# Kernel tuning notes

Hardware: AMD Instinct MI355X
Metric: run time of the kernel (lower is better)

## Reference

```python
import jax, jax.numpy as jnp
import numpy as np
from jax import lax

KSIZE = 3
SIGMA = 0.3 * ((KSIZE - 1) * 0.5 - 1) + 0.8  # cv2 auto-sigma for k=3 -> 0.8

def _gauss_kernel(k, sigma):
    ax = np.arange(k, dtype=np.float64) - (k - 1) / 2
    xx, yy = np.meshgrid(ax, ax, indexing='ij')
    ker = np.exp(-(xx ** 2 + yy ** 2) / (2.0 * sigma ** 2))
    ker /= ker.sum()
    return jnp.asarray(ker, jnp.float32)

SCHARR_X = jnp.array([[-3., 0., 3.], [-10., 0., 10.], [-3., 0., 3.]], jnp.float32)
SCHARR_Y = SCHARR_X.T  # cv2.Scharr(dy=1)

def _conv2d_reflect(img, ker):
    # img: [B,1,H,W]; cross-correlation (like cv2.filter2D) with BORDER_REFLECT_101
    p = ker.shape[0] // 2
    img = jnp.pad(img, ((0, 0), (0, 0), (p, p), (p, p)), mode='reflect')
    return lax.conv_general_dilated(img, ker[None, None], (1, 1), 'VALID')

def setup_inputs() -> dict:
    key = jax.random.key(0)
    x = jax.random.uniform(key, (8, 3, 1024, 1024), dtype=jnp.float32) * 255.0
    return {"x": x}

def reference(x):
    B, C, H, W = x.shape
    # cv2 RGB2GRAY weights
    rgb_w = jnp.array([0.299, 0.587, 0.114], dtype=x.dtype)
    gray = jnp.einsum('bchw,c->bhw', x, rgb_w)[:, None]  # [B,1,H,W]
    blurred = _conv2d_reflect(gray, _gauss_kernel(KSIZE, SIGMA))
    sx = _conv2d_reflect(blurred, SCHARR_X)
    sy = _conv2d_reflect(blurred, SCHARR_Y)
    mag = jnp.sqrt(sx * sx + sy * sy)  # L2_gradient=True
    # forward returns gradient magnitude replicated across channels
    return jnp.broadcast_to(mag, (B, C, H, W))
```

## Files before the change

### kernel.cpp

```cpp
#include <hip/hip_runtime.h>
#include <math.h>


#define IMG_H 1024
#define IMG_W 1024
#define TW 128
#define TH 16
#define GCOLS 136
#define ITEMS 768

#define W0 0.52201125f
#define W1 0.23899437f
#define AV0 0.71698311f
#define AV1 3.95597745f
#define AV2 6.65407872f

typedef float vf4 __attribute__((ext_vector_type(4)));
#define AS_GLOBAL const __attribute__((address_space(1))) void*
#define AS_LDS __attribute__((address_space(3))) void*

__device__ __forceinline__ int reflect101(int v, int n) {
    v = (v < 0) ? -v : v;
    return (v >= n) ? (2 * n - 2 - v) : v;
}

__global__ __launch_bounds__(256, 4)
void edge_kernel(const float* __restrict__ in, float* __restrict__ out) {
    __shared__ __align__(16) float sR[ITEMS * 4];
    __shared__ __align__(16) float sG[ITEMS * 4];
    __shared__ __align__(16) float sB[ITEMS * 4];

    const int tid = threadIdx.x;
    const int bx = blockIdx.x, by = blockIdx.y, b = blockIdx.z;
    const int x0 = bx * TW, y0 = by * TH;

    const size_t plane = (size_t)IMG_H * IMG_W;
    const float* pr = in + (size_t)b * 3 * plane;
    const float* pg = pr + plane;
    const float* pb = pg + plane;

    #pragma unroll
    for (int k = 0; k < 3; ++k) {
        const int item = tid + k * 256;
        const int gy = item / 34;
        const int g4 = (item - gy * 34) * 4;
        const int y = reflect101(y0 - 2 + gy, IMG_H);
        int x = x0 - 4 + g4;
        x = x < 0 ? 0 : (x > IMG_W - 4 ? IMG_W - 4 : x);
        const size_t o = (size_t)y * IMG_W + x;
        __builtin_amdgcn_global_load_lds((AS_GLOBAL)(pr + o), (AS_LDS)&sR[item * 4], 16, 0, 0);
        __builtin_amdgcn_global_load_lds((AS_GLOBAL)(pg + o), (AS_LDS)&sG[item * 4], 16, 0, 0);
        __builtin_amdgcn_global_load_lds((AS_GLOBAL)(pb + o), (AS_LDS)&sB[item * 4], 16, 0, 0);
    }
    __syncthreads();

    #pragma unroll
    for (int k = 0; k < 3; ++k) {
        const int i4 = (tid + k * 256) * 4;
        float4 r = *(const float4*)&sR[i4];
        float4 g = *(const float4*)&sG[i4];
        float4 bb = *(const float4*)&sB[i4];
        float4 gr;
        gr.x = 0.299f * r.x + 0.587f * g.x + 0.114f * bb.x;
        gr.y = 0.299f * r.y + 0.587f * g.y + 0.114f * bb.y;
        gr.z = 0.299f * r.z + 0.587f * g.z + 0.114f * bb.z;
        gr.w = 0.299f * r.w + 0.587f * g.w + 0.114f * bb.w;
        *(float4*)&sR[i4] = gr;
    }
    __syncthreads();

    const int tx = tid & 31;
    const int tyg = tid >> 5;
    const int c4 = tx * 4;
    const int r0 = tyg * 2;
    const bool eBL = (bx == 0) && (tx == 0);
    const bool eBR = (bx == (IMG_W / TW - 1)) && (tx == 31);

    float hs[6][4], hd[6][4];
    #pragma unroll
    for (int s = 0; s < 6; ++s) {
        const float* row = &sR[(r0 + s) * GCOLS + c4];
        float4 ga = *(const float4*)(row);
        float4 gb = *(const float4*)(row + 4);
        float4 gc = *(const float4*)(row + 8);
        float g[12] = {ga.x, ga.y, ga.z, ga.w, gb.x, gb.y, gb.z, gb.w,
                       gc.x, gc.y, gc.z, gc.w};
        if (eBL) { g[2] = g[6]; g[3] = g[5]; }
        if (eBR) { g[8] = g[6]; g[9] = g[5]; }
        #pragma unroll
        for (int k = 0; k < 4; ++k) {
            hs[s][k] = AV0 * (g[k+2] + g[k+6]) + AV1 * (g[k+3] + g[k+5]) + AV2 * g[k+4];
            hd[s][k] = W1 * (g[k+6] - g[k+2]) + W0 * (g[k+5] - g[k+3]);
        }
    }

    float* po = out + (size_t)b * 3 * plane;
    #pragma unroll
    for (int t = 0; t < 2; ++t) {
        vf4 mag;
        #pragma unroll
        for (int k = 0; k < 4; ++k) {
            float sx = AV0 * (hd[t][k] + hd[t+4][k]) + AV1 * (hd[t+1][k] + hd[t+3][k]) + AV2 * hd[t+2][k];
            float sy = W1 * (hs[t+4][k] - hs[t][k]) + W0 * (hs[t+3][k] - hs[t+1][k]);
            mag[k] = sqrtf(sx * sx + sy * sy);
        }
        const size_t o = (size_t)(y0 + r0 + t) * IMG_W + (x0 + c4);
        __builtin_nontemporal_store(mag, (vf4*)(po + o));
        __builtin_nontemporal_store(mag, (vf4*)(po + o + plane));
        __builtin_nontemporal_store(mag, (vf4*)(po + o + 2 * plane));
    }
}

extern "C" void kernel_launch(void* const* d_in, const int* in_sizes, int n_in,
                              void* d_out, int out_size, void* d_ws, size_t ws_size,
                              hipStream_t stream) {
    const float* in = (const float*)d_in[0];
    float* out = (float*)d_out;
    const int B = in_sizes[0] / (3 * IMG_H * IMG_W);
    dim3 grid(IMG_W / TW, IMG_H / TH, B);
    edge_kernel<<<grid, dim3(256), 0, stream>>>(in, out);
}
```

Before: 175.4 us.

## Make blocks persistent over 8 row tiles with double-buffered async LDS staging

```diff
diff --git a/kernel.cpp b/kernel.cpp
--- a/kernel.cpp
+++ b/kernel.cpp
@@ -6,6 +6,7 @@
 #define IMG_W 1024
 #define TW 128
 #define TH 16
+#define NT 8
 #define GCOLS 136
 #define ITEMS 768
 
@@ -24,50 +25,36 @@
     return (v >= n) ? (2 * n - 2 - v) : v;
 }
 
-__global__ __launch_bounds__(256, 4)
+__global__ __launch_bounds__(256, 2)
 void edge_kernel(const float* __restrict__ in, float* __restrict__ out) {
-    __shared__ __align__(16) float sR[ITEMS * 4];
-    __shared__ __align__(16) float sG[ITEMS * 4];
-    __shared__ __align__(16) float sB[ITEMS * 4];
+    __shared__ __align__(16) float sAll[2][3][ITEMS * 4];
 
     const int tid = threadIdx.x;
-    const int bx = blockIdx.x, by = blockIdx.y, b = blockIdx.z;
-    const int x0 = bx * TW, y0 = by * TH;
+    const int bx = blockIdx.x, sy = blockIdx.y, b = blockIdx.z;
+    const int x0 = bx * TW;
+    const int ybase = sy * (TH * NT);
 
     const size_t plane = (size_t)IMG_H * IMG_W;
     const float* pr = in + (size_t)b * 3 * plane;
     const float* pg = pr + plane;
     const float* pb = pg + plane;
+    float* po = out + (size_t)b * 3 * plane;
 
-    #pragma unroll
-    for (int k = 0; k < 3; ++k) {
-        const int item = tid + k * 256;
-        const int gy = item / 34;
-        const int g4 = (item - gy * 34) * 4;
-        const int y = reflect101(y0 - 2 + gy, IMG_H);
-        int x = x0 - 4 + g4;
-        x = x < 0 ? 0 : (x > IMG_W - 4 ? IMG_W - 4 : x);
-        const size_t o = (size_t)y * IMG_W + x;
-        __builtin_amdgcn_global_load_lds((AS_GLOBAL)(pr + o), (AS_LDS)&sR[item * 4], 16, 0, 0);
-        __builtin_amdgcn_global_load_lds((AS_GLOBAL)(pg + o), (AS_LDS)&sG[item * 4], 16, 0, 0);
-        __builtin_amdgcn_global_load_lds((AS_GLOBAL)(pb + o), (AS_LDS)&sB[item * 4], 16, 0, 0);
-    }
-    __syncthreads();
-
-    #pragma unroll
-    for (int k = 0; k < 3; ++k) {
-        const int i4 = (tid + k * 256) * 4;
-        float4 r = *(const float4*)&sR[i4];
-        float4 g = *(const float4*)&sG[i4];
-        float4 bb = *(const float4*)&sB[i4];
-        float4 gr;
-        gr.x = 0.299f * r.x + 0.587f * g.x + 0.114f * bb.x;
-        gr.y = 0.299f * r.y + 0.587f * g.y + 0.114f * bb.y;
-        gr.z = 0.299f * r.z + 0.587f * g.z + 0.114f * bb.z;
-        gr.w = 0.299f * r.w + 0.587f * g.w + 0.114f * bb.w;
-        *(float4*)&sR[i4] = gr;
-    }
-    __syncthreads();
+    auto STAGE = [&](int bufi, int ty0) {
+        #pragma unroll
+        for (int k = 0; k < 3; ++k) {
+            const int item = tid + k * 256;
+            const int gy = item / 34;
+            const int g4 = (item - gy * 34) * 4;
+            const int y = reflect101(ty0 - 2 + gy, IMG_H);
+            int x = x0 - 4 + g4;
+            x = x < 0 ? 0 : (x > IMG_W - 4 ? IMG_W - 4 : x);
+            const size_t o = (size_t)y * IMG_W + x;
+            __builtin_amdgcn_global_load_lds((AS_GLOBAL)(pr + o), (AS_LDS)&sAll[bufi][0][item * 4], 16, 0, 0);
+            __builtin_amdgcn_global_load_lds((AS_GLOBAL)(pg + o), (AS_LDS)&sAll[bufi][1][item * 4], 16, 0, 0);
+            __builtin_amdgcn_global_load_lds((AS_GLOBAL)(pb + o), (AS_LDS)&sAll[bufi][2][item * 4], 16, 0, 0);
+        }
+    };
 
     const int tx = tid & 31;
     const int tyg = tid >> 5;
@@ -76,38 +63,70 @@
     const bool eBL = (bx == 0) && (tx == 0);
     const bool eBR = (bx == (IMG_W / TW - 1)) && (tx == 31);
 
-    float hs[6][4], hd[6][4];
+    STAGE(0, ybase);
+
     #pragma unroll
-    for (int s = 0; s < 6; ++s) {
-        const float* row = &sR[(r0 + s) * GCOLS + c4];
-        float4 ga = *(const float4*)(row);
-        float4 gb = *(const float4*)(row + 4);
-        float4 gc = *(const float4*)(row + 8);
-        float g[12] = {ga.x, ga.y, ga.z, ga.w, gb.x, gb.y, gb.z, gb.w,
-                       gc.x, gc.y, gc.z, gc.w};
-        if (eBL) { g[2] = g[6]; g[3] = g[5]; }
-        if (eBR) { g[8] = g[6]; g[9] = g[5]; }
+    for (int t = 0; t < NT; ++t) {
+        const int cur = t & 1;
+        if (t < NT - 1) STAGE(cur ^ 1, ybase + (t + 1) * TH);
+
+        if (t == 0)            asm volatile("s_waitcnt vmcnt(9)"  ::: "memory");
+        else if (t == NT - 1)  asm volatile("s_waitcnt vmcnt(6)"  ::: "memory");
+        else                   asm volatile("s_waitcnt vmcnt(15)" ::: "memory");
+
         #pragma unroll
-        for (int k = 0; k < 4; ++k) {
-            hs[s][k] = AV0 * (g[k+2] + g[k+6]) + AV1 * (g[k+3] + g[k+5]) + AV2 * g[k+4];
-            hd[s][k] = W1 * (g[k+6] - g[k+2]) + W0 * (g[k+5] - g[k+3]);
+        for (int k = 0; k < 3; ++k) {
+            const int i4 = (tid + k * 256) * 4;
+            float4 r  = *(const float4*)&sAll[cur][0][i4];
+            float4 g  = *(const float4*)&sAll[cur][1][i4];
+            float4 bb = *(const float4*)&sAll[cur][2][i4];
+            float4 gr;
+            gr.x = 0.299f * r.x + 0.587f * g.x + 0.114f * bb.x;
+            gr.y = 0.299f * r.y + 0.587f * g.y + 0.114f * bb.y;
+            gr.z = 0.299f * r.z + 0.587f * g.z + 0.114f * bb.z;
+            gr.w = 0.299f * r.w + 0.587f * g.w + 0.114f * bb.w;
+            *(float4*)&sAll[cur][0][i4] = gr;
         }
-    }
+        asm volatile("s_waitcnt lgkmcnt(0)" ::: "memory");
+        __builtin_amdgcn_s_barrier();
+        __builtin_amdgcn_sched_barrier(0);
 
-    float* po = out + (size_t)b * 3 * plane;
-    #pragma unroll
-    for (int t = 0; t < 2; ++t) {
-        vf4 mag;
+        const int ty0 = ybase + t * TH;
+        float hs[6][4], hd[6][4];
         #pragma unroll
-        for (int k = 0; k < 4; ++k) {
-            float sx = AV0 * (hd[t][k] + hd[t+4][k]) + AV1 * (hd[t+1][k] + hd[t+3][k]) + AV2 * hd[t+2][k];
-            float sy = W1 * (hs[t+4][k] - hs[t][k]) + W0 * (hs[t+3][k] - hs[t+1][k]);
-            mag[k] = sqrtf(sx * sx + sy * sy);
+        for (int s = 0; s < 6; ++s) {
+            const float* row = &sAll[cur][0][(r0 + s) * GCOLS + c4];
+            float4 ga = *(const float4*)(row);
+            float4 gb = *(const float4*)(row + 4);
+            float4 gc = *(const float4*)(row + 8);
+            float g[12] = {ga.x, ga.y, ga.z, ga.w, gb.x, gb.y, gb.z, gb.w,
+                           gc.x, gc.y, gc.z, gc.w};
+            if (eBL) { g[2] = g[6]; g[3] = g[5]; }
+            if (eBR) { g[8] = g[6]; g[9] = g[5]; }
+            #pragma unroll
+            for (int k = 0; k < 4; ++k) {
+                hs[s][k] = AV0 * (g[k+2] + g[k+6]) + AV1 * (g[k+3] + g[k+5]) + AV2 * g[k+4];
+                hd[s][k] = W1 * (g[k+6] - g[k+2]) + W0 * (g[k+5] - g[k+3]);
+            }
         }
-        const size_t o = (size_t)(y0 + r0 + t) * IMG_W + (x0 + c4);
-        __builtin_nontemporal_store(mag, (vf4*)(po + o));
-        __builtin_nontemporal_store(mag, (vf4*)(po + o + plane));
-        __builtin_nontemporal_store(mag, (vf4*)(po + o + 2 * plane));
+
+        #pragma unroll
+        for (int t2 = 0; t2 < 2; ++t2) {
+            vf4 mag;
+            #pragma unroll
+            for (int k = 0; k < 4; ++k) {
+                float sx = AV0 * (hd[t2][k] + hd[t2+4][k]) + AV1 * (hd[t2+1][k] + hd[t2+3][k]) + AV2 * hd[t2+2][k];
+                float sy2 = W1 * (hs[t2+4][k] - hs[t2][k]) + W0 * (hs[t2+3][k] - hs[t2+1][k]);
+                mag[k] = sqrtf(sx * sx + sy2 * sy2);
+            }
+            const size_t o = (size_t)(ty0 + r0 + t2) * IMG_W + (x0 + c4);
+            __builtin_nontemporal_store(mag, (vf4*)(po + o));
+            __builtin_nontemporal_store(mag, (vf4*)(po + o + plane));
+            __builtin_nontemporal_store(mag, (vf4*)(po + o + 2 * plane));
+        }
+
+        __builtin_amdgcn_s_barrier();
+        __builtin_amdgcn_sched_barrier(0);
     }
 }
 
@@ -117,6 +136,6 @@
     const float* in = (const float*)d_in[0];
     float* out = (float*)d_out;
     const int B = in_sizes[0] / (3 * IMG_H * IMG_W);
-    dim3 grid(IMG_W / TW, IMG_H / TH, B);
+    dim3 grid(IMG_W / TW, IMG_H / (TH * NT), B);
     edge_kernel<<<grid, dim3(256), 0, stream>>>(in, out);
 }
```

Measured after the change: 185.6 us. +5.8%, slower.

## Replace LDS tiling with register rows and wavefront shuffles for halo exchange

Applied to the files above, without the earlier changes.

```diff
diff --git a/kernel.cpp b/kernel.cpp
--- a/kernel.cpp
+++ b/kernel.cpp
@@ -4,10 +4,6 @@
 
 #define IMG_H 1024
 #define IMG_W 1024
-#define TW 128
-#define TH 16
-#define GCOLS 136
-#define ITEMS 768
 
 #define W0 0.52201125f
 #define W1 0.23899437f
@@ -16,85 +12,94 @@
 #define AV2 6.65407872f
 
 typedef float vf4 __attribute__((ext_vector_type(4)));
-#define AS_GLOBAL const __attribute__((address_space(1))) void*
-#define AS_LDS __attribute__((address_space(3))) void*
 
 __device__ __forceinline__ int reflect101(int v, int n) {
     v = (v < 0) ? -v : v;
     return (v >= n) ? (2 * n - 2 - v) : v;
 }
 
+__device__ __forceinline__ float grayf(float r, float g, float b) {
+    return 0.299f * r + 0.587f * g + 0.114f * b;
+}
+
 __global__ __launch_bounds__(256, 4)
 void edge_kernel(const float* __restrict__ in, float* __restrict__ out) {
-    __shared__ __align__(16) float sR[ITEMS * 4];
-    __shared__ __align__(16) float sG[ITEMS * 4];
-    __shared__ __align__(16) float sB[ITEMS * 4];
-
-    const int tid = threadIdx.x;
-    const int bx = blockIdx.x, by = blockIdx.y, b = blockIdx.z;
-    const int x0 = bx * TW, y0 = by * TH;
+    const int lane = threadIdx.x & 63;
+    const int wv   = threadIdx.x >> 6;
+    const int bx   = blockIdx.x;
+    const int strip = (bx & 7) * 64 + (bx >> 3);
+    const int b    = blockIdx.y;
+    const int y0   = strip * 2;
+    const int x4   = wv * 256 + lane * 4;
 
     const size_t plane = (size_t)IMG_H * IMG_W;
     const float* pr = in + (size_t)b * 3 * plane;
     const float* pg = pr + plane;
     const float* pb = pg + plane;
+    float* po = out + (size_t)b * 3 * plane;
 
+    const bool eL = (lane == 0), eR = (lane == 63);
+    const bool eAny = eL || eR;
+    const bool trueL = eL && (x4 == 0);
+    const bool trueR = eR && (x4 == IMG_W - 4);
+    const int hx = eR ? (x4 + 4 > IMG_W - 4 ? IMG_W - 4 : x4 + 4)
+                      : (x4 - 4 < 0 ? 0 : x4 - 4);
+
+    float4 cR[6], cG[6], cB[6];
+    float4 hR[6], hG[6], hB[6];
+    int yy[6];
     #pragma unroll
-    for (int k = 0; k < 3; ++k) {
-        const int item = tid + k * 256;
-        const int gy = item / 34;
-        const int g4 = (item - gy * 34) * 4;
-        const int y = reflect101(y0 - 2 + gy, IMG_H);
-        int x = x0 - 4 + g4;
-        x = x < 0 ? 0 : (x > IMG_W - 4 ? IMG_W - 4 : x);
-        const size_t o = (size_t)y * IMG_W + x;
-        __builtin_amdgcn_global_load_lds((AS_GLOBAL)(pr + o), (AS_LDS)&sR[item * 4], 16, 0, 0);
-        __builtin_amdgcn_global_load_lds((AS_GLOBAL)(pg + o), (AS_LDS)&sG[item * 4], 16, 0, 0);
-        __builtin_amdgcn_global_load_lds((AS_GLOBAL)(pb + o), (AS_LDS)&sB[item * 4], 16, 0, 0);
+    for (int r = 0; r < 6; ++r) {
+        yy[r] = reflect101(y0 - 2 + r, IMG_H);
+        const size_t o = (size_t)yy[r] * IMG_W + x4;
+        cR[r] = *(const float4*)(pr + o);
+        cG[r] = *(const float4*)(pg + o);
+        cB[r] = *(const float4*)(pb + o);
     }
-    __syncthreads();
-
-    #pragma unroll
-    for (int k = 0; k < 3; ++k) {
-        const int i4 = (tid + k * 256) * 4;
-        float4 r = *(const float4*)&sR[i4];
-        float4 g = *(const float4*)&sG[i4];
-        float4 bb = *(const float4*)&sB[i4];
-        float4 gr;
-        gr.x = 0.299f * r.x + 0.587f * g.x + 0.114f * bb.x;
-        gr.y = 0.299f * r.y + 0.587f * g.y + 0.114f * bb.y;
-        gr.z = 0.299f * r.z + 0.587f * g.z + 0.114f * bb.z;
-        gr.w = 0.299f * r.w + 0.587f * g.w + 0.114f * bb.w;
-        *(float4*)&sR[i4] = gr;
+    if (eAny) {
+        #pragma unroll
+        for (int r = 0; r < 6; ++r) {
+            const size_t o = (size_t)yy[r] * IMG_W + hx;
+            hR[r] = *(const float4*)(pr + o);
+            hG[r] = *(const float4*)(pg + o);
+            hB[r] = *(const float4*)(pb + o);
+        }
     }
-    __syncthreads();
-
-    const int tx = tid & 31;
-    const int tyg = tid >> 5;
-    const int c4 = tx * 4;
-    const int r0 = tyg * 2;
-    const bool eBL = (bx == 0) && (tx == 0);
-    const bool eBR = (bx == (IMG_W / TW - 1)) && (tx == 31);
 
     float hs[6][4], hd[6][4];
     #pragma unroll
-    for (int s = 0; s < 6; ++s) {
-        const float* row = &sR[(r0 + s) * GCOLS + c4];
-        float4 ga = *(const float4*)(row);
-        float4 gb = *(const float4*)(row + 4);
-        float4 gc = *(const float4*)(row + 8);
-        float g[12] = {ga.x, ga.y, ga.z, ga.w, gb.x, gb.y, gb.z, gb.w,
-                       gc.x, gc.y, gc.z, gc.w};
-        if (eBL) { g[2] = g[6]; g[3] = g[5]; }
-        if (eBR) { g[8] = g[6]; g[9] = g[5]; }
-        #pragma unroll
-        for (int k = 0; k < 4; ++k) {
-            hs[s][k] = AV0 * (g[k+2] + g[k+6]) + AV1 * (g[k+3] + g[k+5]) + AV2 * g[k+4];
-            hd[s][k] = W1 * (g[k+6] - g[k+2]) + W0 * (g[k+5] - g[k+3]);
+    for (int r = 0; r < 6; ++r) {
+        float g0 = grayf(cR[r].x, cG[r].x, cB[r].x);
+        float g1 = grayf(cR[r].y, cG[r].y, cB[r].y);
+        float g2 = grayf(cR[r].z, cG[r].z, cB[r].z);
+        float g3 = grayf(cR[r].w, cG[r].w, cB[r].w);
+        float lm2 = __shfl_up(g2, 1);
+        float lm1 = __shfl_up(g3, 1);
+        float rp4 = __shfl_down(g0, 1);
+        float rp5 = __shfl_down(g1, 1);
+        if (eAny) {
+            float h0 = grayf(hR[r].x, hG[r].x, hB[r].x);
+            float h1 = grayf(hR[r].y, hG[r].y, hB[r].y);
+            float h2 = grayf(hR[r].z, hG[r].z, hB[r].z);
+            float h3 = grayf(hR[r].w, hG[r].w, hB[r].w);
+            if (eL) {
+                lm2 = h2;
+                lm1 = trueL ? h1 : h3;
+            } else {
+                rp4 = trueR ? h2 : h0;
+                rp5 = h1;
+            }
         }
+        hs[r][0] = AV0 * (lm2 + g2) + AV1 * (lm1 + g1) + AV2 * g0;
+        hs[r][1] = AV0 * (lm1 + g3) + AV1 * (g0 + g2) + AV2 * g1;
+        hs[r][2] = AV0 * (g0 + rp4) + AV1 * (g1 + g3) + AV2 * g2;
+        hs[r][3] = AV0 * (g1 + rp5) + AV1 * (g2 + rp4) + AV2 * g3;
+        hd[r][0] = W1 * (g2 - lm2) + W0 * (g1 - lm1);
+        hd[r][1] = W1 * (g3 - lm1) + W0 * (g2 - g0);
+        hd[r][2] = W1 * (rp4 - g0) + W0 * (g3 - g1);
+        hd[r][3] = W1 * (rp5 - g1) + W0 * (rp4 - g2);
     }
 
-    float* po = out + (size_t)b * 3 * plane;
     #pragma unroll
     for (int t = 0; t < 2; ++t) {
         vf4 mag;
@@ -104,7 +109,7 @@
             float sy = W1 * (hs[t+4][k] - hs[t][k]) + W0 * (hs[t+3][k] - hs[t+1][k]);
             mag[k] = sqrtf(sx * sx + sy * sy);
         }
-        const size_t o = (size_t)(y0 + r0 + t) * IMG_W + (x0 + c4);
+        const size_t o = (size_t)(y0 + t) * IMG_W + x4;
         __builtin_nontemporal_store(mag, (vf4*)(po + o));
         __builtin_nontemporal_store(mag, (vf4*)(po + o + plane));
         __builtin_nontemporal_store(mag, (vf4*)(po + o + 2 * plane));
@@ -117,6 +122,6 @@
     const float* in = (const float*)d_in[0];
     float* out = (float*)d_out;
     const int B = in_sizes[0] / (3 * IMG_H * IMG_W);
-    dim3 grid(IMG_W / TW, IMG_H / TH, B);
+    dim3 grid(IMG_H / 2, B);
     edge_kernel<<<grid, dim3(256), 0, stream>>>(in, out);
 }
```

After: 246.4 us. +40.5%, slower.
